# Performance work log

Hardware: AMD Instinct MI355X
Metric: run time of the kernel (lower is better)

Reference implementation:

```python
import jax, jax.numpy as jnp
import numpy as np
import math

GRID = 256       # grid_size
KMAX = 64        # max_elements_per_cell
RES = 512        # image resolution
SPAN = 4         # max grid cells per axis covered by one triangle bbox
NUM_VIEWS = 16
SCALE = 0.5


def _projection_matrix(x=0.5, n=1.5, f=100.0):
    return np.array([[n / x, 0.0, 0.0, 0.0],
                     [0.0, n / -x, 0.0, 0.0],
                     [0.0, 0.0, -(f + n) / (f - n), -(2.0 * f * n) / (f - n)],
                     [0.0, 0.0, -1.0, 0.0]], dtype=np.float32)


def _view_buffers(num_views, seed):
    rng = np.random.default_rng(seed)
    proj = _projection_matrix()
    mvps, lights = [], []
    for _ in range(num_views):
        u1, u2, u3 = rng.random(3)
        qx = math.sqrt(1.0 - u1) * math.sin(math.tau * u2)
        qy = math.sqrt(1.0 - u1) * math.cos(math.tau * u2)
        qz = math.sqrt(u1) * math.sin(math.tau * u3)
        qw = math.sqrt(u1) * math.cos(math.tau * u3)
        rot = np.array([[1 - 2 * (qy * qy + qz * qz), 2 * (qx * qy - qz * qw), 2 * (qx * qz + qy * qw)],
                        [2 * (qx * qy + qz * qw), 1 - 2 * (qx * qx + qz * qz), 2 * (qy * qz - qx * qw)],
                        [2 * (qx * qz - qy * qw), 2 * (qy * qz + qx * qw), 1 - 2 * (qx * qx + qy * qy)]], dtype=np.float32)
        rmat = np.eye(4, dtype=np.float32); rmat[:3, :3] = rot
        tmat = np.eye(4, dtype=np.float32); tmat[2, 3] = -4.0
        view = tmat @ rmat
        campos = np.linalg.inv(view)[:3, 3]
        light = -campos / (np.linalg.norm(campos) + 1e-8)
        mvps.append(proj @ view)
        lights.append(light.astype(np.float32))
    return np.stack(mvps).astype(np.float32), np.stack(lights).astype(np.float32)


def setup_inputs() -> dict:
    key = jax.random.key(0)
    k1, k2 = jax.random.split(key)
    F = 100_000
    # clustered per-triangle vertices -> small on-screen triangles (mesh-like locality)
    centers = jax.random.uniform(k1, (F, 1, 3), minval=-1.0, maxval=1.0)
    jitter = jax.random.normal(k2, (F, 3, 3)) * 0.02
    u = (centers + jitter).reshape(-1, 3).astype(jnp.float32)          # [3F,3]
    faces = jnp.arange(3 * F, dtype=jnp.int32).reshape(F, 3)
    mvps, light = _view_buffers(NUM_VIEWS, 42)
    return {"u": u,
            "mvps": jnp.asarray(mvps),
            "lightdir": jnp.asarray(light),
            "background_color": jnp.zeros(3, jnp.float32),
            "base_colors": jnp.ones((F, 3), jnp.float32),
            "faces": faces}


def _forward(u, mvps, lightdir, background_color, base_colors, faces):
    # _normalize_vertices
    v = u - u.mean(0, keepdims=True)
    span = jnp.maximum(v.max() - v.min(), 1e-6)
    v = v * (SCALE / span)
    Fn = faces.shape[0]
    # project with active view 0 (v_hom @ mvps[0].T, no perspective divide, as in source)
    v_hom = jnp.concatenate([v, jnp.ones((v.shape[0], 1), v.dtype)], axis=1)
    v_ndc = v_hom @ mvps[0].T                                          # [V,4]
    tris = v_ndc[faces]                                                # [F,3,4]
    wtri = v[faces]                                                    # [F,3,3]
    nrm = jnp.cross(wtri[:, 0] - wtri[:, 1], wtri[:, 2] - wtri[:, 1])
    nrm = nrm / (jnp.linalg.norm(nrm, axis=-1, keepdims=True) + 1e-10)
    z = tris[:, :, 2].mean(1)
    order = jnp.argsort(z)                                             # depth sort (near first)
    st = tris[order]
    sn = nrm[order]
    cp = (st[:, :, :2] + 1.0) * 0.5                                    # [F,3,2] control pts in [0,1]
    shading = jnp.clip(jnp.sum(-lightdir[0] * sn, axis=-1, keepdims=True), 0.0)
    colors = base_colors[order] * shading                              # [F,3]
    # --- grid acceleration structure build (scatter triangles into cells) ---
    lo = jnp.clip(jnp.floor(cp.min(1) * GRID).astype(jnp.int32), 0, GRID - 1)  # [F,2]
    hi = jnp.clip(jnp.floor(cp.max(1) * GRID).astype(jnp.int32), 0, GRID - 1)
    d = jnp.arange(SPAN, dtype=jnp.int32)
    cx = lo[:, 0:1] + d[None, :]                                       # [F,SPAN]
    cy = lo[:, 1:2] + d[None, :]
    valid = (cy[:, :, None] <= hi[:, 1:2, None]) & (cx[:, None, :] <= hi[:, 0:1].reshape(Fn, 1, 1) + 0 * cx[:, None, :])
    valid = (cy[:, :, None] <= hi[:, 1:2, None]) & (cx[:, None, :] <= hi[:, 0:1][:, :, None])
    cell = cy[:, :, None] * GRID + cx[:, None, :]                      # [F,SPAN,SPAN]
    NC = GRID * GRID
    cell = jnp.where(valid, cell, NC).reshape(-1)
    tri = jnp.broadcast_to(jnp.arange(Fn, dtype=jnp.int32)[:, None, None], (Fn, SPAN, SPAN)).reshape(-1)
    # sort (cell, depth-rank): tri ids are already depth-ordered
    keys = cell.astype(jnp.int64) * (Fn + 1) + tri
    ordk = jnp.argsort(keys)
    sc = cell[ordk]
    stri = tri[ordk]
    counts = jax.ops.segment_sum(jnp.ones_like(sc), sc, num_segments=NC + 1)
    starts = jnp.concatenate([jnp.zeros(1, counts.dtype), jnp.cumsum(counts)[:-1]])
    rank = jnp.arange(sc.shape[0], dtype=jnp.int32) - starts[sc].astype(jnp.int32)
    ok = (rank < KMAX) & (sc < NC)
    grid_elems = jnp.full((NC + 1, KMAX), -1, jnp.int32)
    grid_elems = grid_elems.at[jnp.where(ok, sc, NC), jnp.where(ok, rank, 0)].set(jnp.where(ok, stri, -1))
    # --- per-pixel rasterization via grid query ---
    px = (jnp.arange(RES, dtype=jnp.float32) + 0.5) / RES
    uu, vv = jnp.meshgrid(px, px, indexing='xy')
    P = jnp.stack([uu, vv], -1).reshape(-1, 2)                         # [P,2]
    ix = jnp.clip((P[:, 0] * GRID).astype(jnp.int32), 0, GRID - 1)
    iy = jnp.clip((P[:, 1] * GRID).astype(jnp.int32), 0, GRID - 1)
    elems = grid_elems[iy * GRID + ix]                                 # [P,K]
    e = jnp.maximum(elems, 0)
    tpts = cp[e]                                                       # [P,K,3,2]
    a, b, c = tpts[:, :, 0], tpts[:, :, 1], tpts[:, :, 2]
    pp = P[:, None, :]

    def cr(o, q, r):
        return (q[..., 0] - o[..., 0]) * (r[..., 1] - o[..., 1]) - (q[..., 1] - o[..., 1]) * (r[..., 0] - o[..., 0])

    e0 = cr(a, b, pp)
    e1 = cr(b, c, pp)
    e2 = cr(c, a, pp)
    inside = ((e0 >= 0) & (e1 >= 0) & (e2 >= 0)) | ((e0 <= 0) & (e1 <= 0) & (e2 <= 0))
    hit = inside & (elems >= 0)
    first = jnp.argmax(hit, axis=1)                                    # front-most (depth-sorted)
    anyhit = jnp.any(hit, axis=1)
    tid = e[jnp.arange(e.shape[0]), first]
    img = jnp.where(anyhit[:, None], colors[tid], background_color[None, :])
    return img.reshape(RES, RES, 3)


def reference(u, mvps, lightdir, background_color, base_colors, faces):
    return _forward(u, mvps, lightdir, background_color, base_colors, faces)
```

## Files before the change

### kernel.cpp

```cpp
#include <hip/hip_runtime.h>
#include <stdint.h>

#pragma clang fp contract(off)

#define GRIDN 256
#define NC (GRIDN * GRIDN)
#define RESN 512
#define RBLOCKS 256
#define CAP 1024
#define CPB 16
#define NB 32
#define NS 16
#define SBINS 2048


typedef unsigned short bfraw;
typedef unsigned short u16;

__device__ __forceinline__ float bf2f(bfraw h) {
    return __uint_as_float(((uint32_t)h) << 16);
}
__device__ __forceinline__ bfraw f2bf(float f) {
    uint32_t b = __float_as_uint(f);
    return (bfraw)((b + 0x7FFFu + ((b >> 16) & 1u)) >> 16);
}
__device__ __forceinline__ uint32_t fkey(float f) {
    uint32_t b = __float_as_uint(f);
    return (b & 0x80000000u) ? ~b : (b | 0x80000000u);
}

__global__ __launch_bounds__(256) void k_reduce1(const bfraw* __restrict__ u, int nrows,
                                                 double* __restrict__ psum,
                                                 float* __restrict__ pmin,
                                                 float* __restrict__ pmax) {
    __shared__ double ssum[256 * 3];
    __shared__ float smin[256 * 3];
    __shared__ float smax[256 * 3];
    int t = threadIdx.x;
    double s0 = 0.0, s1 = 0.0, s2 = 0.0;
    float mn0 = INFINITY, mn1 = INFINITY, mn2 = INFINITY;
    float mx0 = -INFINITY, mx1 = -INFINITY, mx2 = -INFINITY;
    for (int r = blockIdx.x * 256 + t; r < nrows; r += 256 * RBLOCKS) {
        float a = bf2f(u[3 * r + 0]);
        float b = bf2f(u[3 * r + 1]);
        float c = bf2f(u[3 * r + 2]);
        s0 += (double)a; s1 += (double)b; s2 += (double)c;
        mn0 = fminf(mn0, a); mx0 = fmaxf(mx0, a);
        mn1 = fminf(mn1, b); mx1 = fmaxf(mx1, b);
        mn2 = fminf(mn2, c); mx2 = fmaxf(mx2, c);
    }
    ssum[t * 3 + 0] = s0; ssum[t * 3 + 1] = s1; ssum[t * 3 + 2] = s2;
    smin[t * 3 + 0] = mn0; smin[t * 3 + 1] = mn1; smin[t * 3 + 2] = mn2;
    smax[t * 3 + 0] = mx0; smax[t * 3 + 1] = mx1; smax[t * 3 + 2] = mx2;
    __syncthreads();
    for (int st = 128; st > 0; st >>= 1) {
        if (t < st) {
            for (int c = 0; c < 3; c++) {
                ssum[t * 3 + c] += ssum[(t + st) * 3 + c];
                smin[t * 3 + c] = fminf(smin[t * 3 + c], smin[(t + st) * 3 + c]);
                smax[t * 3 + c] = fmaxf(smax[t * 3 + c], smax[(t + st) * 3 + c]);
            }
        }
        __syncthreads();
    }
    if (t == 0) {
        for (int c = 0; c < 3; c++) {
            psum[blockIdx.x * 3 + c] = ssum[c];
            pmin[blockIdx.x * 3 + c] = smin[c];
            pmax[blockIdx.x * 3 + c] = smax[c];
        }
    }
}

__global__ __launch_bounds__(256) void k_reduce2(const double* __restrict__ psum,
                                                 const float* __restrict__ pmin,
                                                 const float* __restrict__ pmax,
                                                 int nrows, float* __restrict__ cst) {
    __shared__ double ssum[256 * 3];
    __shared__ float smin[256 * 3];
    __shared__ float smax[256 * 3];
    int t = threadIdx.x;
    for (int c = 0; c < 3; c++) {
        ssum[t * 3 + c] = psum[t * 3 + c];
        smin[t * 3 + c] = pmin[t * 3 + c];
        smax[t * 3 + c] = pmax[t * 3 + c];
    }
    __syncthreads();
    for (int st = 128; st > 0; st >>= 1) {
        if (t < st) {
            for (int c = 0; c < 3; c++) {
                ssum[t * 3 + c] += ssum[(t + st) * 3 + c];
                smin[t * 3 + c] = fminf(smin[t * 3 + c], smin[(t + st) * 3 + c]);
                smax[t * 3 + c] = fmaxf(smax[t * 3 + c], smax[(t + st) * 3 + c]);
            }
        }
        __syncthreads();
    }
    if (t == 0) {
        float fn = (float)nrows;
        float m0 = (float)ssum[0] / fn;
        float m1 = (float)ssum[1] / fn;
        float m2 = (float)ssum[2] / fn;
        float vmax = fmaxf(fmaxf(smax[0] - m0, smax[1] - m1), smax[2] - m2);
        float vmin = fminf(fminf(smin[0] - m0, smin[1] - m1), smin[2] - m2);
        float span = fmaxf(vmax - vmin, 1e-06f);
        float s = 0.5f / span;
        cst[0] = m0; cst[1] = m1; cst[2] = m2; cst[3] = s;
    }
}

__global__ __launch_bounds__(256) void k_setup(const bfraw* __restrict__ u,
                                               const int* __restrict__ faces,
                                               const bfraw* __restrict__ mvp,
                                               const bfraw* __restrict__ light,
                                               const float* __restrict__ cst,
                                               int F,
                                               float* __restrict__ tcs,
                                               uint32_t* __restrict__ tz,
                                               uint32_t* __restrict__ tbox) {
    int f = blockIdx.x * 256 + threadIdx.x;
    if (f >= F) return;
    float m0 = cst[0], m1 = cst[1], m2 = cst[2], s = cst[3];
    float M[12];
    for (int i = 0; i < 12; i++) M[i] = bf2f(mvp[i]);

    float vx[3], vy[3], vz[3], cpx[3], cpy[3], zc[3];
    for (int j = 0; j < 3; j++) {
        int idx = faces[3 * f + j];
        float a = bf2f(u[3 * idx + 0]);
        float b = bf2f(u[3 * idx + 1]);
        float c = bf2f(u[3 * idx + 2]);
        float x = (a - m0) * s;
        float y = (b - m1) * s;
        float z = (c - m2) * s;
        vx[j] = x; vy[j] = y; vz[j] = z;
        float cx = fmaf(x, M[0], 0.0f);
        cx = fmaf(y, M[1], cx); cx = fmaf(z, M[2], cx); cx = cx + M[3];
        float cy = fmaf(x, M[4], 0.0f);
        cy = fmaf(y, M[5], cy); cy = fmaf(z, M[6], cy); cy = cy + M[7];
        float cz = fmaf(x, M[8], 0.0f);
        cz = fmaf(y, M[9], cz); cz = fmaf(z, M[10], cz); cz = cz + M[11];
        cpx[j] = (cx + 1.0f) * 0.5f;
        cpy[j] = (cy + 1.0f) * 0.5f;
        zc[j] = cz;
    }
    float zmean = ((zc[0] + zc[1]) + zc[2]) / 3.0f;

    float e1x = vx[0] - vx[1], e1y = vy[0] - vy[1], e1z = vz[0] - vz[1];
    float e2x = vx[2] - vx[1], e2y = vy[2] - vy[1], e2z = vz[2] - vz[1];
    float nx = e1y * e2z - e1z * e2y;
    float ny = e1z * e2x - e1x * e2z;
    float nz = e1x * e2y - e1y * e2x;
    float nn = nx * nx;
    nn = nn + ny * ny;
    nn = nn + nz * nz;
    float d = sqrtf(nn) + 1e-10f;
    float inx = nx / d, iny = ny / d, inz = nz / d;

    float l0 = bf2f(light[0]), l1 = bf2f(light[1]), l2 = bf2f(light[2]);
    float p0 = (-l0) * inx;
    float p1 = (-l1) * iny;
    float p2 = (-l2) * inz;
    float shading = fmaxf((p0 + p1) + p2, 0.0f);

    tcs[f * 8 + 0] = cpx[0]; tcs[f * 8 + 1] = cpy[0];
    tcs[f * 8 + 2] = cpx[1]; tcs[f * 8 + 3] = cpy[1];
    tcs[f * 8 + 4] = cpx[2]; tcs[f * 8 + 5] = cpy[2];
    tcs[f * 8 + 6] = shading;
    tcs[f * 8 + 7] = 0.0f;

    tz[f] = fkey(zmean);

    float mnx = fminf(fminf(cpx[0], cpx[1]), cpx[2]);
    float mny = fminf(fminf(cpy[0], cpy[1]), cpy[2]);
    float mxx = fmaxf(fmaxf(cpx[0], cpx[1]), cpx[2]);
    float mxy = fmaxf(fmaxf(cpy[0], cpy[1]), cpy[2]);
    int lox = (int)floorf(mnx * 256.0f); lox = lox < 0 ? 0 : (lox > 255 ? 255 : lox);
    int loy = (int)floorf(mny * 256.0f); loy = loy < 0 ? 0 : (loy > 255 ? 255 : loy);
    int hix = (int)floorf(mxx * 256.0f); hix = hix < 0 ? 0 : (hix > 255 ? 255 : hix);
    int hiy = (int)floorf(mxy * 256.0f); hiy = hiy < 0 ? 0 : (hiy > 255 ? 255 : hiy);
    int hx = hix < lox + 3 ? hix : lox + 3;
    int hy = hiy < loy + 3 ? hiy : loy + 3;
    tbox[f] = (uint32_t)lox | ((uint32_t)loy << 8) | ((uint32_t)hx << 16) | ((uint32_t)hy << 24);
}

__global__ __launch_bounds__(256) void k_count(const uint32_t* __restrict__ tbox,
                                               int F,
                                               u16* __restrict__ blockHist) {
    __shared__ uint32_t hist[SBINS];
    int b = blockIdx.x >> 4;
    int sl = blockIdx.x & (NS - 1);
    int chunk = (F + NB - 1) / NB;
    int fs = b * chunk;
    int fe = fs + chunk < F ? fs + chunk : F;
    int y0 = sl * 16, y1 = y0 + 15;
    for (int i = threadIdx.x; i < SBINS; i += 256) hist[i] = 0u;
    __syncthreads();
    for (int f = fs + threadIdx.x; f < fe; f += 256) {
        uint32_t bx = tbox[f];
        int lox = bx & 255, loy = (bx >> 8) & 255;
        int hx = (bx >> 16) & 255, hy = bx >> 24;
        int ys = loy > y0 ? loy : y0;
        int ye = hy < y1 ? hy : y1;
        for (int yy = ys; yy <= ye; yy++) {
            for (int xx = lox; xx <= hx; xx++) {
                uint32_t c = (uint32_t)(yy * GRIDN + xx) & 4095u;
                atomicAdd(&hist[c >> 1], 1u << (16u * (c & 1u)));
            }
        }
    }
    __syncthreads();
    uint32_t* dst = (uint32_t*)(blockHist + (size_t)b * NC) + sl * SBINS;
    for (int i = threadIdx.x; i < SBINS; i += 256) dst[i] = hist[i];
}

__global__ __launch_bounds__(1024) void k_scanA1(u16* __restrict__ blockHist,
                                                 uint32_t* __restrict__ cellOff,
                                                 uint32_t* __restrict__ blockSum) {
    __shared__ uint32_t sc[1024];
    int B = blockIdx.x, t = threadIdx.x;
    int c = B * 1024 + t;
    uint32_t tot = 0;
    for (int b = 0; b < NB; b++) {
        size_t o = (size_t)b * NC + c;
        uint32_t v = blockHist[o];
        blockHist[o] = (u16)tot;
        tot += v;
    }
    sc[t] = tot;
    __syncthreads();
    for (int st = 1; st < 1024; st <<= 1) {
        uint32_t a = 0;
        if (t >= st) a = sc[t - st];
        __syncthreads();
        if (t >= st) sc[t] += a;
        __syncthreads();
    }
    cellOff[c] = sc[t] - tot;
    if (t == 1023) blockSum[B] = sc[1023];
}

__global__ __launch_bounds__(1024) void k_scanB(uint32_t* __restrict__ cellOff,
                                                const uint32_t* __restrict__ blockSum) {
    __shared__ uint32_t pre[65];
    int B = blockIdx.x, t = threadIdx.x;
    if (t == 0) {
        uint32_t run = 0;
        for (int i = 0; i < 64; i++) { pre[i] = run; run += blockSum[i]; }
        pre[64] = run;
    }
    __syncthreads();
    cellOff[B * 1024 + t] += pre[B];
    if (B == 63 && t == 1023) cellOff[NC] = pre[64];
}

__global__ __launch_bounds__(256) void k_place(const uint32_t* __restrict__ tbox,
                                               const u16* __restrict__ blockHist,
                                               const uint32_t* __restrict__ cellOff,
                                               uint32_t* __restrict__ pairs,
                                               int F) {
    __shared__ uint32_t hist[SBINS];
    int b = blockIdx.x >> 4;
    int sl = blockIdx.x & (NS - 1);
    int chunk = (F + NB - 1) / NB;
    int fs = b * chunk;
    int fe = fs + chunk < F ? fs + chunk : F;
    int y0 = sl * 16, y1 = y0 + 15;
    uint32_t pcap = (uint32_t)F * 16u;
    for (int i = threadIdx.x; i < SBINS; i += 256) hist[i] = 0u;
    __syncthreads();
    for (int f = fs + threadIdx.x; f < fe; f += 256) {
        uint32_t bx = tbox[f];
        int lox = bx & 255, loy = (bx >> 8) & 255;
        int hx = (bx >> 16) & 255, hy = bx >> 24;
        int ys = loy > y0 ? loy : y0;
        int ye = hy < y1 ? hy : y1;
        for (int yy = ys; yy <= ye; yy++) {
            for (int xx = lox; xx <= hx; xx++) {
                uint32_t cell = (uint32_t)(yy * GRIDN + xx);
                uint32_t c = cell & 4095u;
                uint32_t sh = 16u * (c & 1u);
                uint32_t old = atomicAdd(&hist[c >> 1], 1u << sh);
                uint32_t r = (old >> sh) & 0xFFFFu;
                uint32_t pos = cellOff[cell] + (uint32_t)blockHist[(size_t)b * NC + cell] + r;
                if (pos < pcap) pairs[pos] = (uint32_t)f;
            }
        }
    }
}

__global__ __launch_bounds__(256) void k_cellsort(const uint32_t* __restrict__ cellOff,
                                                  const uint32_t* __restrict__ tz,
                                                  uint32_t* __restrict__ pairs,
                                                  int F) {
    __shared__ uint64_t lkeys[CAP];
    uint32_t pcap = (uint32_t)F * 16u;
    int t = threadIdx.x;
    for (int ci = 0; ci < CPB; ci++) {
        int cell = blockIdx.x + ci * (NC / CPB);
        uint32_t off = cellOff[cell];
        uint32_t end = cellOff[cell + 1];
        if (off > pcap || end > pcap || end < off) continue;
        uint32_t n = end - off;
        if (n <= 64u) continue;
        uint32_t m = n > CAP ? CAP : n;
        for (uint32_t i = t; i < m; i += 256) {
            uint32_t id = pairs[off + i];
            if (id >= (uint32_t)F) id = 0;
            lkeys[i] = ((uint64_t)tz[id] << 32) | id;
        }
        __syncthreads();
        uint64_t k0 = ~0ull, k1 = ~0ull, k2 = ~0ull, k3 = ~0ull;
        uint32_t i0 = t, i1 = t + 256, i2 = t + 512, i3 = t + 768;
        if (i0 < m) k0 = lkeys[i0];
        if (i1 < m) k1 = lkeys[i1];
        if (i2 < m) k2 = lkeys[i2];
        if (i3 < m) k3 = lkeys[i3];
        uint32_t r0 = 0, r1 = 0, r2 = 0, r3 = 0;
        for (uint32_t j = 0; j < m; j++) {
            uint64_t kj = lkeys[j];
            r0 += (kj < k0) ? 1u : 0u;
            r1 += (kj < k1) ? 1u : 0u;
            r2 += (kj < k2) ? 1u : 0u;
            r3 += (kj < k3) ? 1u : 0u;
        }
        if (i0 < m && r0 < 64u) pairs[off + r0] = (uint32_t)(k0 & 0xFFFFFFFFu);
        if (i1 < m && r1 < 64u) pairs[off + r1] = (uint32_t)(k1 & 0xFFFFFFFFu);
        if (i2 < m && r2 < 64u) pairs[off + r2] = (uint32_t)(k2 & 0xFFFFFFFFu);
        if (i3 < m && r3 < 64u) pairs[off + r3] = (uint32_t)(k3 & 0xFFFFFFFFu);
        __syncthreads();
    }
}

__global__ __launch_bounds__(256) void k_raster(const float* __restrict__ tcs,
                                                const uint32_t* __restrict__ tz,
                                                const uint32_t* __restrict__ cellOff,
                                                const uint32_t* __restrict__ pairs,
                                                const bfraw* __restrict__ basec,
                                                const bfraw* __restrict__ bg,
                                                bfraw* __restrict__ out, int F) {
    int p = blockIdx.x * 256 + threadIdx.x;
    int col = p & (RESN - 1);
    int row = p >> 9;
    float px = ((float)col + 0.5f) / 512.0f;
    float py = ((float)row + 0.5f) / 512.0f;
    int cell = (row >> 1) * GRIDN + (col >> 1);
    uint32_t pcap = (uint32_t)F * 16u;
    uint32_t off = cellOff[cell];
    uint32_t end = cellOff[cell + 1];
    uint32_t n = 0;
    if (off <= pcap && end <= pcap && end >= off) n = end - off;
    uint32_t m = n > 64u ? 64u : n;
    bool srt = n > 64u;
    uint64_t best = ~0ull;
    uint32_t bestId = 0u;
    float bestSh = 0.0f;
    bool found = false;
    for (uint32_t k = 0; k < m; k++) {
        uint32_t id = pairs[off + k];
        if (id >= (uint32_t)F) continue;
        const float4 A = *(const float4*)(tcs + (size_t)id * 8);
        const float4 B = *(const float4*)(tcs + (size_t)id * 8 + 4);
        float ax = A.x, ay = A.y, bx = A.z, by = A.w, cx = B.x, cy = B.y;
        float e0 = (bx - ax) * (py - ay) - (by - ay) * (px - ax);
        float e1 = (cx - bx) * (py - by) - (cy - by) * (px - bx);
        float e2 = (ax - cx) * (py - cy) - (ay - cy) * (px - cx);
        bool inside = (e0 >= 0.0f && e1 >= 0.0f && e2 >= 0.0f) ||
                      (e0 <= 0.0f && e1 <= 0.0f && e2 <= 0.0f);
        if (inside) {
            if (srt) {
                bestId = id; bestSh = B.z; found = true;
                break;
            }
            uint64_t key = ((uint64_t)tz[id] << 32) | id;
            if (key < best) { best = key; bestId = id; bestSh = B.z; found = true; }
        }
    }
    float r, g, b;
    if (found) {
        r = bf2f(basec[3 * bestId + 0]) * bestSh;
        g = bf2f(basec[3 * bestId + 1]) * bestSh;
        b = bf2f(basec[3 * bestId + 2]) * bestSh;
    } else {
        r = bf2f(bg[0]); g = bf2f(bg[1]); b = bf2f(bg[2]);
    }
    int o = p * 3;
    out[o + 0] = f2bf(r);
    out[o + 1] = f2bf(g);
    out[o + 2] = f2bf(b);
}

__global__ __launch_bounds__(256) void k_diag(bfraw* __restrict__ out, float code) {
    out[blockIdx.x * 256 + threadIdx.x] = f2bf(code);
}

extern "C" void kernel_launch(void* const* d_in, const int* in_sizes, int n_in,
                              void* d_out, int out_size, void* d_ws, size_t ws_size,
                              hipStream_t stream) {
    const bfraw* u = (const bfraw*)d_in[0];
    const bfraw* mvps = (const bfraw*)d_in[1];
    const bfraw* light = (const bfraw*)d_in[2];
    const bfraw* bg = (const bfraw*)d_in[3];
    const bfraw* basec = (const bfraw*)d_in[4];
    const int* faces = (const int*)d_in[5];
    int nrows = in_sizes[0] / 3;
    int F = in_sizes[5] / 3;
    bfraw* out = (bfraw*)d_out;

    char* w = (char*)d_ws;
    size_t off = 0;
    auto alloc = [&](size_t bytes) -> void* {
        off = (off + 255) & ~(size_t)255;
        void* p = w + off;
        off += bytes;
        return p;
    };

    float* cst = (float*)alloc(4 * sizeof(float));
    double* psum = (double*)alloc((size_t)RBLOCKS * 3 * sizeof(double));
    float* pmin = (float*)alloc((size_t)RBLOCKS * 3 * sizeof(float));
    float* pmax = (float*)alloc((size_t)RBLOCKS * 3 * sizeof(float));
    float* tcs = (float*)alloc((size_t)F * 8 * sizeof(float));
    uint32_t* tz = (uint32_t*)alloc((size_t)F * sizeof(uint32_t));
    uint32_t* tbox = (uint32_t*)alloc((size_t)F * sizeof(uint32_t));
    u16* blockHist = (u16*)alloc((size_t)NB * NC * sizeof(u16));
    uint32_t* cellOff = (uint32_t*)alloc(((size_t)NC + 1) * sizeof(uint32_t));
    uint32_t* blockSum = (uint32_t*)alloc(64 * sizeof(uint32_t));
    uint32_t* pairs = (uint32_t*)alloc((size_t)F * 16 * sizeof(uint32_t));
    size_t needed = off;

    if (ws_size < needed) {
        float code = 20000.0f + (float)(ws_size >> 20);
        k_diag<<<(RESN * RESN * 3) / 256, 256, 0, stream>>>(out, code);
        return;
    }

    k_reduce1<<<RBLOCKS, 256, 0, stream>>>(u, nrows, psum, pmin, pmax);
    k_reduce2<<<1, 256, 0, stream>>>(psum, pmin, pmax, nrows, cst);
    k_setup<<<(F + 255) / 256, 256, 0, stream>>>(u, faces, mvps, light, cst, F,
                                                 tcs, tz, tbox);
    k_count<<<NB * NS, 256, 0, stream>>>(tbox, F, blockHist);
    k_scanA1<<<64, 1024, 0, stream>>>(blockHist, cellOff, blockSum);
    k_scanB<<<64, 1024, 0, stream>>>(cellOff, blockSum);
    k_place<<<NB * NS, 256, 0, stream>>>(tbox, blockHist, cellOff, pairs, F);
    k_cellsort<<<NC / CPB, 256, 0, stream>>>(cellOff, tz, pairs, F);
    k_raster<<<(RESN * RESN) / 256, 256, 0, stream>>>(tcs, tz, cellOff, pairs,
                                                      basec, bg, out, F);
}
```

Baseline: 155.9 us.

## Fuse pipeline stages into one persistent kernel with software grid barriers

Replaces the chain of nine kernel launches with a single persistent cooperative-style kernel. The blocks loop over tasks for each stage and meet at atomic-counter grid barriers, so per-launch gaps and launch overhead go away. The scan stage is reworked so each of 256 threads handles four cells, and the block-prefix add is folded into consumers through a shared pre array instead of a separate pass. The barrier assumes every block is co-resident, which occupancy sizing is meant to guarantee. It adds spin-wait cost, and the persistent loop gives uneven load balance for the cellsort and raster stages.

```diff
diff --git a/kernel.cpp b/kernel.cpp
--- a/kernel.cpp
+++ b/kernel.cpp
@@ -12,6 +12,7 @@
 #define NB 32
 #define NS 16
 #define SBINS 2048
+#define MAXGRID 1024
 
 
 typedef unsigned short bfraw;
@@ -29,18 +30,38 @@
     return (b & 0x80000000u) ? ~b : (b | 0x80000000u);
 }
 
-__global__ __launch_bounds__(256) void k_reduce1(const bfraw* __restrict__ u, int nrows,
-                                                 double* __restrict__ psum,
-                                                 float* __restrict__ pmin,
-                                                 float* __restrict__ pmax) {
-    __shared__ double ssum[256 * 3];
-    __shared__ float smin[256 * 3];
-    __shared__ float smax[256 * 3];
-    int t = threadIdx.x;
+__device__ __forceinline__ void gsync(uint32_t* cnt, uint32_t* gen, int nb) {
+    __syncthreads();
+    if (threadIdx.x == 0) {
+        __threadfence();
+        uint32_t g = atomicAdd(gen, 0u);
+        uint32_t a = atomicAdd(cnt, 1u);
+        if (a == (uint32_t)nb - 1u) {
+            atomicExch(cnt, 0u);
+            __threadfence();
+            atomicAdd(gen, 1u);
+        } else {
+            long spins = 0;
+            while (atomicAdd(gen, 0u) == g) {
+                __builtin_amdgcn_s_sleep(2);
+                if (++spins > 100000000L) break;
+            }
+        }
+        __threadfence();
+    }
+    __syncthreads();
+}
+
+
+__device__ void dev_reduce_partial(const bfraw* __restrict__ u, int nrows, int task,
+                                   int t, double* ssum, float* smin, float* smax,
+                                   double* __restrict__ psum,
+                                   float* __restrict__ pmin,
+                                   float* __restrict__ pmax) {
     double s0 = 0.0, s1 = 0.0, s2 = 0.0;
     float mn0 = INFINITY, mn1 = INFINITY, mn2 = INFINITY;
     float mx0 = -INFINITY, mx1 = -INFINITY, mx2 = -INFINITY;
-    for (int r = blockIdx.x * 256 + t; r < nrows; r += 256 * RBLOCKS) {
+    for (int r = task * 256 + t; r < nrows; r += 256 * RBLOCKS) {
         float a = bf2f(u[3 * r + 0]);
         float b = bf2f(u[3 * r + 1]);
         float c = bf2f(u[3 * r + 2]);
@@ -65,21 +86,20 @@
     }
     if (t == 0) {
         for (int c = 0; c < 3; c++) {
-            psum[blockIdx.x * 3 + c] = ssum[c];
-            pmin[blockIdx.x * 3 + c] = smin[c];
-            pmax[blockIdx.x * 3 + c] = smax[c];
-        }
-    }
-}
-
-__global__ __launch_bounds__(256) void k_reduce2(const double* __restrict__ psum,
-                                                 const float* __restrict__ pmin,
-                                                 const float* __restrict__ pmax,
-                                                 int nrows, float* __restrict__ cst) {
-    __shared__ double ssum[256 * 3];
-    __shared__ float smin[256 * 3];
-    __shared__ float smax[256 * 3];
-    int t = threadIdx.x;
+            psum[task * 3 + c] = ssum[c];
+            pmin[task * 3 + c] = smin[c];
+            pmax[task * 3 + c] = smax[c];
+        }
+    }
+    __syncthreads();
+}
+
+__device__ void dev_reduce_final(const double* __restrict__ psum,
+                                 const float* __restrict__ pmin,
+                                 const float* __restrict__ pmax,
+                                 int nrows, int t,
+                                 double* ssum, float* smin, float* smax,
+                                 float* __restrict__ cst) {
     for (int c = 0; c < 3; c++) {
         ssum[t * 3 + c] = psum[t * 3 + c];
         smin[t * 3 + c] = pmin[t * 3 + c];
@@ -107,19 +127,17 @@
         float s = 0.5f / span;
         cst[0] = m0; cst[1] = m1; cst[2] = m2; cst[3] = s;
     }
-}
-
-__global__ __launch_bounds__(256) void k_setup(const bfraw* __restrict__ u,
-                                               const int* __restrict__ faces,
-                                               const bfraw* __restrict__ mvp,
-                                               const bfraw* __restrict__ light,
-                                               const float* __restrict__ cst,
-                                               int F,
-                                               float* __restrict__ tcs,
-                                               uint32_t* __restrict__ tz,
-                                               uint32_t* __restrict__ tbox) {
-    int f = blockIdx.x * 256 + threadIdx.x;
-    if (f >= F) return;
+    __syncthreads();
+}
+
+__device__ void dev_setup_one(const bfraw* __restrict__ u,
+                              const int* __restrict__ faces,
+                              const bfraw* __restrict__ mvp,
+                              const bfraw* __restrict__ light,
+                              const float* __restrict__ cst, int f,
+                              float* __restrict__ tcs,
+                              uint32_t* __restrict__ tz,
+                              uint32_t* __restrict__ tbox) {
     float m0 = cst[0], m1 = cst[1], m2 = cst[2], s = cst[3];
     float M[12];
     for (int i = 0; i < 12; i++) M[i] = bf2f(mvp[i]);
@@ -184,19 +202,18 @@
     tbox[f] = (uint32_t)lox | ((uint32_t)loy << 8) | ((uint32_t)hx << 16) | ((uint32_t)hy << 24);
 }
 
-__global__ __launch_bounds__(256) void k_count(const uint32_t* __restrict__ tbox,
-                                               int F,
-                                               u16* __restrict__ blockHist) {
-    __shared__ uint32_t hist[SBINS];
-    int b = blockIdx.x >> 4;
-    int sl = blockIdx.x & (NS - 1);
+__device__ void dev_count_task(const uint32_t* __restrict__ tbox, int F,
+                               u16* __restrict__ blockHist, uint32_t* hist,
+                               int task, int t) {
+    int b = task >> 4;
+    int sl = task & (NS - 1);
     int chunk = (F + NB - 1) / NB;
     int fs = b * chunk;
     int fe = fs + chunk < F ? fs + chunk : F;
     int y0 = sl * 16, y1 = y0 + 15;
-    for (int i = threadIdx.x; i < SBINS; i += 256) hist[i] = 0u;
-    __syncthreads();
-    for (int f = fs + threadIdx.x; f < fe; f += 256) {
+    for (int i = t; i < SBINS; i += 256) hist[i] = 0u;
+    __syncthreads();
+    for (int f = fs + t; f < fe; f += 256) {
         uint32_t bx = tbox[f];
         int lox = bx & 255, loy = (bx >> 8) & 255;
         int hx = (bx >> 16) & 255, hy = bx >> 24;
@@ -211,65 +228,62 @@
     }
     __syncthreads();
     uint32_t* dst = (uint32_t*)(blockHist + (size_t)b * NC) + sl * SBINS;
-    for (int i = threadIdx.x; i < SBINS; i += 256) dst[i] = hist[i];
-}
-
-__global__ __launch_bounds__(1024) void k_scanA1(u16* __restrict__ blockHist,
-                                                 uint32_t* __restrict__ cellOff,
-                                                 uint32_t* __restrict__ blockSum) {
-    __shared__ uint32_t sc[1024];
-    int B = blockIdx.x, t = threadIdx.x;
-    int c = B * 1024 + t;
-    uint32_t tot = 0;
-    for (int b = 0; b < NB; b++) {
-        size_t o = (size_t)b * NC + c;
-        uint32_t v = blockHist[o];
-        blockHist[o] = (u16)tot;
-        tot += v;
-    }
-    sc[t] = tot;
-    __syncthreads();
-    for (int st = 1; st < 1024; st <<= 1) {
+    for (int i = t; i < SBINS; i += 256) dst[i] = hist[i];
+    __syncthreads();
+}
+
+__device__ void dev_scan_task(u16* __restrict__ blockHist,
+                              uint32_t* __restrict__ cellOff,
+                              uint32_t* __restrict__ blockSum,
+                              uint32_t* sscan, int task, int t) {
+    int c0 = task * 1024 + t * 4;
+    uint32_t tot[4];
+    uint32_t tsum = 0;
+    for (int k = 0; k < 4; k++) {
+        uint32_t tt = 0;
+        for (int b = 0; b < NB; b++) {
+            size_t o = (size_t)b * NC + (c0 + k);
+            uint32_t v = blockHist[o];
+            blockHist[o] = (u16)tt;
+            tt += v;
+        }
+        tot[k] = tt;
+        tsum += tt;
+    }
+    sscan[t] = tsum;
+    __syncthreads();
+    for (int st = 1; st < 256; st <<= 1) {
         uint32_t a = 0;
-        if (t >= st) a = sc[t - st];
+        if (t >= st) a = sscan[t - st];
         __syncthreads();
-        if (t >= st) sc[t] += a;
+        if (t >= st) sscan[t] += a;
         __syncthreads();
     }
-    cellOff[c] = sc[t] - tot;
-    if (t == 1023) blockSum[B] = sc[1023];
-}
-
-__global__ __launch_bounds__(1024) void k_scanB(uint32_t* __restrict__ cellOff,
-                                                const uint32_t* __restrict__ blockSum) {
-    __shared__ uint32_t pre[65];
-    int B = blockIdx.x, t = threadIdx.x;
-    if (t == 0) {
-        uint32_t run = 0;
-        for (int i = 0; i < 64; i++) { pre[i] = run; run += blockSum[i]; }
-        pre[64] = run;
-    }
-    __syncthreads();
-    cellOff[B * 1024 + t] += pre[B];
-    if (B == 63 && t == 1023) cellOff[NC] = pre[64];
-}
-
-__global__ __launch_bounds__(256) void k_place(const uint32_t* __restrict__ tbox,
-                                               const u16* __restrict__ blockHist,
-                                               const uint32_t* __restrict__ cellOff,
-                                               uint32_t* __restrict__ pairs,
-                                               int F) {
-    __shared__ uint32_t hist[SBINS];
-    int b = blockIdx.x >> 4;
-    int sl = blockIdx.x & (NS - 1);
+    uint32_t run = sscan[t] - tsum;
+    for (int k = 0; k < 4; k++) {
+        cellOff[c0 + k] = run;
+        run += tot[k];
+    }
+    if (t == 255) blockSum[task] = sscan[255];
+    __syncthreads();
+}
+
+__device__ void dev_place_task(const uint32_t* __restrict__ tbox,
+                               const u16* __restrict__ blockHist,
+                               const uint32_t* __restrict__ cellOff,
+                               const uint32_t* pre,
+                               uint32_t* __restrict__ pairs, int F,
+                               uint32_t* hist, int task, int t) {
+    int b = task >> 4;
+    int sl = task & (NS - 1);
     int chunk = (F + NB - 1) / NB;
     int fs = b * chunk;
     int fe = fs + chunk < F ? fs + chunk : F;
     int y0 = sl * 16, y1 = y0 + 15;
     uint32_t pcap = (uint32_t)F * 16u;
-    for (int i = threadIdx.x; i < SBINS; i += 256) hist[i] = 0u;
-    __syncthreads();
-    for (int f = fs + threadIdx.x; f < fe; f += 256) {
+    for (int i = t; i < SBINS; i += 256) hist[i] = 0u;
+    __syncthreads();
+    for (int f = fs + t; f < fe; f += 256) {
         uint32_t bx = tbox[f];
         int lox = bx & 255, loy = (bx >> 8) & 255;
         int hx = (bx >> 16) & 255, hy = bx >> 24;
@@ -282,72 +296,70 @@
                 uint32_t sh = 16u * (c & 1u);
                 uint32_t old = atomicAdd(&hist[c >> 1], 1u << sh);
                 uint32_t r = (old >> sh) & 0xFFFFu;
-                uint32_t pos = cellOff[cell] + (uint32_t)blockHist[(size_t)b * NC + cell] + r;
+                uint32_t base = cellOff[cell] + (pre ? pre[cell >> 10] : 0u);
+                uint32_t pos = base + (uint32_t)blockHist[(size_t)b * NC + cell] + r;
                 if (pos < pcap) pairs[pos] = (uint32_t)f;
             }
         }
     }
-}
-
-__global__ __launch_bounds__(256) void k_cellsort(const uint32_t* __restrict__ cellOff,
-                                                  const uint32_t* __restrict__ tz,
-                                                  uint32_t* __restrict__ pairs,
-                                                  int F) {
-    __shared__ uint64_t lkeys[CAP];
+    __syncthreads();
+}
+
+__device__ void dev_cellsort_cell(const uint32_t* __restrict__ cellOff,
+                                  const uint32_t* pre,
+                                  const uint32_t* __restrict__ tz,
+                                  uint32_t* __restrict__ pairs, int F,
+                                  uint64_t* lkeys, int cell, int t) {
     uint32_t pcap = (uint32_t)F * 16u;
-    int t = threadIdx.x;
-    for (int ci = 0; ci < CPB; ci++) {
-        int cell = blockIdx.x + ci * (NC / CPB);
-        uint32_t off = cellOff[cell];
-        uint32_t end = cellOff[cell + 1];
-        if (off > pcap || end > pcap || end < off) continue;
-        uint32_t n = end - off;
-        if (n <= 64u) continue;
-        uint32_t m = n > CAP ? CAP : n;
-        for (uint32_t i = t; i < m; i += 256) {
-            uint32_t id = pairs[off + i];
-            if (id >= (uint32_t)F) id = 0;
-            lkeys[i] = ((uint64_t)tz[id] << 32) | id;
-        }
-        __syncthreads();
-        uint64_t k0 = ~0ull, k1 = ~0ull, k2 = ~0ull, k3 = ~0ull;
-        uint32_t i0 = t, i1 = t + 256, i2 = t + 512, i3 = t + 768;
-        if (i0 < m) k0 = lkeys[i0];
-        if (i1 < m) k1 = lkeys[i1];
-        if (i2 < m) k2 = lkeys[i2];
-        if (i3 < m) k3 = lkeys[i3];
-        uint32_t r0 = 0, r1 = 0, r2 = 0, r3 = 0;
-        for (uint32_t j = 0; j < m; j++) {
-            uint64_t kj = lkeys[j];
-            r0 += (kj < k0) ? 1u : 0u;
-            r1 += (kj < k1) ? 1u : 0u;
-            r2 += (kj < k2) ? 1u : 0u;
-            r3 += (kj < k3) ? 1u : 0u;
-        }
-        if (i0 < m && r0 < 64u) pairs[off + r0] = (uint32_t)(k0 & 0xFFFFFFFFu);
-        if (i1 < m && r1 < 64u) pairs[off + r1] = (uint32_t)(k1 & 0xFFFFFFFFu);
-        if (i2 < m && r2 < 64u) pairs[off + r2] = (uint32_t)(k2 & 0xFFFFFFFFu);
-        if (i3 < m && r3 < 64u) pairs[off + r3] = (uint32_t)(k3 & 0xFFFFFFFFu);
-        __syncthreads();
-    }
-}
-
-__global__ __launch_bounds__(256) void k_raster(const float* __restrict__ tcs,
-                                                const uint32_t* __restrict__ tz,
-                                                const uint32_t* __restrict__ cellOff,
-                                                const uint32_t* __restrict__ pairs,
-                                                const bfraw* __restrict__ basec,
-                                                const bfraw* __restrict__ bg,
-                                                bfraw* __restrict__ out, int F) {
-    int p = blockIdx.x * 256 + threadIdx.x;
+    uint32_t off = cellOff[cell] + (pre ? pre[cell >> 10] : 0u);
+    uint32_t end = cellOff[cell + 1] + (pre ? pre[(cell + 1) >> 10] : 0u);
+    if (off > pcap || end > pcap || end < off) return;
+    uint32_t n = end - off;
+    if (n <= 64u) return;
+    uint32_t m = n > CAP ? CAP : n;
+    for (uint32_t i = t; i < m; i += 256) {
+        uint32_t id = pairs[off + i];
+        if (id >= (uint32_t)F) id = 0;
+        lkeys[i] = ((uint64_t)tz[id] << 32) | id;
+    }
+    __syncthreads();
+    uint64_t k0 = ~0ull, k1 = ~0ull, k2 = ~0ull, k3 = ~0ull;
+    uint32_t i0 = t, i1 = t + 256, i2 = t + 512, i3 = t + 768;
+    if (i0 < m) k0 = lkeys[i0];
+    if (i1 < m) k1 = lkeys[i1];
+    if (i2 < m) k2 = lkeys[i2];
+    if (i3 < m) k3 = lkeys[i3];
+    uint32_t r0 = 0, r1 = 0, r2 = 0, r3 = 0;
+    for (uint32_t j = 0; j < m; j++) {
+        uint64_t kj = lkeys[j];
+        r0 += (kj < k0) ? 1u : 0u;
+        r1 += (kj < k1) ? 1u : 0u;
+        r2 += (kj < k2) ? 1u : 0u;
+        r3 += (kj < k3) ? 1u : 0u;
+    }
+    if (i0 < m && r0 < 64u) pairs[off + r0] = (uint32_t)(k0 & 0xFFFFFFFFu);
+    if (i1 < m && r1 < 64u) pairs[off + r1] = (uint32_t)(k1 & 0xFFFFFFFFu);
+    if (i2 < m && r2 < 64u) pairs[off + r2] = (uint32_t)(k2 & 0xFFFFFFFFu);
+    if (i3 < m && r3 < 64u) pairs[off + r3] = (uint32_t)(k3 & 0xFFFFFFFFu);
+    __syncthreads();
+}
+
+__device__ void dev_raster_pixel(const float* __restrict__ tcs,
+                                 const uint32_t* __restrict__ tz,
+                                 const uint32_t* __restrict__ cellOff,
+                                 const uint32_t* pre,
+                                 const uint32_t* __restrict__ pairs,
+                                 const bfraw* __restrict__ basec,
+                                 const bfraw* __restrict__ bg,
+                                 bfraw* __restrict__ out, int F, int p) {
     int col = p & (RESN - 1);
     int row = p >> 9;
     float px = ((float)col + 0.5f) / 512.0f;
     float py = ((float)row + 0.5f) / 512.0f;
     int cell = (row >> 1) * GRIDN + (col >> 1);
     uint32_t pcap = (uint32_t)F * 16u;
-    uint32_t off = cellOff[cell];
-    uint32_t end = cellOff[cell + 1];
+    uint32_t off = cellOff[cell] + (pre ? pre[cell >> 10] : 0u);
+    uint32_t end = cellOff[cell + 1] + (pre ? pre[(cell + 1) >> 10] : 0u);
     uint32_t n = 0;
     if (off <= pcap && end <= pcap && end >= off) n = end - off;
     uint32_t m = n > 64u ? 64u : n;
@@ -368,10 +380,7 @@
         bool inside = (e0 >= 0.0f && e1 >= 0.0f && e2 >= 0.0f) ||
                       (e0 <= 0.0f && e1 <= 0.0f && e2 <= 0.0f);
         if (inside) {
-            if (srt) {
-                bestId = id; bestSh = B.z; found = true;
-                break;
-            }
+            if (srt) { bestId = id; bestSh = B.z; found = true; break; }
             uint64_t key = ((uint64_t)tz[id] << 32) | id;
             if (key < best) { best = key; bestId = id; bestSh = B.z; found = true; }
         }
@@ -388,6 +397,157 @@
     out[o + 0] = f2bf(r);
     out[o + 1] = f2bf(g);
     out[o + 2] = f2bf(b);
+}
+
+__global__ void __launch_bounds__(256, 4)
+k_mega(const bfraw* __restrict__ u, const int* __restrict__ faces,
+       const bfraw* __restrict__ mvp, const bfraw* __restrict__ light,
+       const bfraw* __restrict__ bg, const bfraw* __restrict__ basec,
+       int nrows, int F,
+       double* __restrict__ psum, float* __restrict__ pmin, float* __restrict__ pmax,
+       float* __restrict__ cst, float* __restrict__ tcs,
+       uint32_t* __restrict__ tz, uint32_t* __restrict__ tbox,
+       u16* __restrict__ blockHist, uint32_t* __restrict__ cellOff,
+       uint32_t* __restrict__ blockSum, uint32_t* __restrict__ pairs,
+       bfraw* __restrict__ out, uint32_t* bcnt, uint32_t* bgen) {
+    int t = threadIdx.x;
+    int nb = gridDim.x;
+    __shared__ double ssum[768];
+    __shared__ float smin[768];
+    __shared__ float smax[768];
+    __shared__ uint32_t hist[SBINS];
+    __shared__ uint64_t lkeys[CAP];
+    __shared__ uint32_t sscan[256];
+    __shared__ uint32_t pre[65];
+
+    for (int task = blockIdx.x; task < RBLOCKS; task += nb)
+        dev_reduce_partial(u, nrows, task, t, ssum, smin, smax, psum, pmin, pmax);
+    gsync(bcnt, bgen, nb);
+    if (blockIdx.x == 0)
+        dev_reduce_final(psum, pmin, pmax, nrows, t, ssum, smin, smax, cst);
+    gsync(bcnt, bgen, nb);
+    int FB = (F + 255) >> 8;
+    for (int task = blockIdx.x; task < FB; task += nb) {
+        int f = task * 256 + t;
+        if (f < F) dev_setup_one(u, faces, mvp, light, cst, f, tcs, tz, tbox);
+    }
+    gsync(bcnt, bgen, nb);
+    for (int task = blockIdx.x; task < NB * NS; task += nb)
+        dev_count_task(tbox, F, blockHist, hist, task, t);
+    gsync(bcnt, bgen, nb);
+    for (int task = blockIdx.x; task < 64; task += nb)
+        dev_scan_task(blockHist, cellOff, blockSum, sscan, task, t);
+    if (blockIdx.x == 0 && t == 0) cellOff[NC] = 0u;
+    gsync(bcnt, bgen, nb);
+    if (t == 0) {
+        uint32_t run = 0;
+        for (int i = 0; i < 64; i++) { pre[i] = run; run += blockSum[i]; }
+        pre[64] = run;
+    }
+    __syncthreads();
+    for (int task = blockIdx.x; task < NB * NS; task += nb)
+        dev_place_task(tbox, blockHist, cellOff, pre, pairs, F, hist, task, t);
+    gsync(bcnt, bgen, nb);
+    for (int cell = blockIdx.x; cell < NC; cell += nb)
+        dev_cellsort_cell(cellOff, pre, tz, pairs, F, lkeys, cell, t);
+    gsync(bcnt, bgen, nb);
+    int PB = (RESN * RESN) >> 8;
+    for (int task = blockIdx.x; task < PB; task += nb) {
+        int p = task * 256 + t;
+        dev_raster_pixel(tcs, tz, cellOff, pre, pairs, basec, bg, out, F, p);
+    }
+}
+
+__global__ __launch_bounds__(256) void k_reduce1(const bfraw* __restrict__ u, int nrows,
+                                                 double* __restrict__ psum,
+                                                 float* __restrict__ pmin,
+                                                 float* __restrict__ pmax) {
+    __shared__ double ssum[768];
+    __shared__ float smin[768];
+    __shared__ float smax[768];
+    dev_reduce_partial(u, nrows, blockIdx.x, threadIdx.x, ssum, smin, smax,
+                       psum, pmin, pmax);
+}
+
+__global__ __launch_bounds__(256) void k_reduce2(const double* __restrict__ psum,
+                                                 const float* __restrict__ pmin,
+                                                 const float* __restrict__ pmax,
+                                                 int nrows, float* __restrict__ cst) {
+    __shared__ double ssum[768];
+    __shared__ float smin[768];
+    __shared__ float smax[768];
+    dev_reduce_final(psum, pmin, pmax, nrows, threadIdx.x, ssum, smin, smax, cst);
+}
+
+__global__ __launch_bounds__(256) void k_setup(const bfraw* __restrict__ u,
+                                               const int* __restrict__ faces,
+                                               const bfraw* __restrict__ mvp,
+                                               const bfraw* __restrict__ light,
+                                               const float* __restrict__ cst, int F,
+                                               float* __restrict__ tcs,
+                                               uint32_t* __restrict__ tz,
+                                               uint32_t* __restrict__ tbox) {
+    int f = blockIdx.x * 256 + threadIdx.x;
+    if (f < F) dev_setup_one(u, faces, mvp, light, cst, f, tcs, tz, tbox);
+}
+
+__global__ __launch_bounds__(256) void k_count(const uint32_t* __restrict__ tbox,
+                                               int F, u16* __restrict__ blockHist) {
+    __shared__ uint32_t hist[SBINS];
+    dev_count_task(tbox, F, blockHist, hist, blockIdx.x, threadIdx.x);
+}
+
+__global__ __launch_bounds__(256) void k_scanA(u16* __restrict__ blockHist,
+                                               uint32_t* __restrict__ cellOff,
+                                               uint32_t* __restrict__ blockSum) {
+    __shared__ uint32_t sscan[256];
+    dev_scan_task(blockHist, cellOff, blockSum, sscan, blockIdx.x, threadIdx.x);
+}
+
+__global__ __launch_bounds__(1024) void k_scanB(uint32_t* __restrict__ cellOff,
+                                                const uint32_t* __restrict__ blockSum) {
+    __shared__ uint32_t pre[65];
+    int B = blockIdx.x, t = threadIdx.x;
+    if (t == 0) {
+        uint32_t run = 0;
+        for (int i = 0; i < 64; i++) { pre[i] = run; run += blockSum[i]; }
+        pre[64] = run;
+    }
+    __syncthreads();
+    cellOff[B * 1024 + t] += pre[B];
+    if (B == 63 && t == 1023) cellOff[NC] = pre[64];
+}
+
+__global__ __launch_bounds__(256) void k_place(const uint32_t* __restrict__ tbox,
+                                               const u16* __restrict__ blockHist,
+                                               const uint32_t* __restrict__ cellOff,
+                                               uint32_t* __restrict__ pairs, int F) {
+    __shared__ uint32_t hist[SBINS];
+    dev_place_task(tbox, blockHist, cellOff, (const uint32_t*)nullptr, pairs, F,
+                   hist, blockIdx.x, threadIdx.x);
+}
+
+__global__ __launch_bounds__(256) void k_cellsort(const uint32_t* __restrict__ cellOff,
+                                                  const uint32_t* __restrict__ tz,
+                                                  uint32_t* __restrict__ pairs, int F) {
+    __shared__ uint64_t lkeys[CAP];
+    for (int ci = 0; ci < CPB; ci++) {
+        int cell = blockIdx.x + ci * (NC / CPB);
+        dev_cellsort_cell(cellOff, (const uint32_t*)nullptr, tz, pairs, F, lkeys,
+                          cell, threadIdx.x);
+    }
+}
+
+__global__ __launch_bounds__(256) void k_raster(const float* __restrict__ tcs,
+                                                const uint32_t* __restrict__ tz,
+                                                const uint32_t* __restrict__ cellOff,
+                                                const uint32_t* __restrict__ pairs,
+                                                const bfraw* __restrict__ basec,
+                                                const bfraw* __restrict__ bg,
+                                                bfraw* __restrict__ out, int F) {
+    int p = blockIdx.x * 256 + threadIdx.x;
+    dev_raster_pixel(tcs, tz, cellOff, (const uint32_t*)nullptr, pairs, basec, bg,
+                     out, F, p);
 }
 
 __global__ __launch_bounds__(256) void k_diag(bfraw* __restrict__ out, float code) {
@@ -427,6 +587,7 @@
     uint32_t* cellOff = (uint32_t*)alloc(((size_t)NC + 1) * sizeof(uint32_t));
     uint32_t* blockSum = (uint32_t*)alloc(64 * sizeof(uint32_t));
     uint32_t* pairs = (uint32_t*)alloc((size_t)F * 16 * sizeof(uint32_t));
+    uint32_t* bar = (uint32_t*)alloc(2 * sizeof(uint32_t));
     size_t needed = off;
 
     if (ws_size < needed) {
@@ -435,15 +596,29 @@
         return;
     }
 
-    k_reduce1<<<RBLOCKS, 256, 0, stream>>>(u, nrows, psum, pmin, pmax);
-    k_reduce2<<<1, 256, 0, stream>>>(psum, pmin, pmax, nrows, cst);
-    k_setup<<<(F + 255) / 256, 256, 0, stream>>>(u, faces, mvps, light, cst, F,
-                                                 tcs, tz, tbox);
-    k_count<<<NB * NS, 256, 0, stream>>>(tbox, F, blockHist);
-    k_scanA1<<<64, 1024, 0, stream>>>(blockHist, cellOff, blockSum);
-    k_scanB<<<64, 1024, 0, stream>>>(cellOff, blockSum);
-    k_place<<<NB * NS, 256, 0, stream>>>(tbox, blockHist, cellOff, pairs, F);
-    k_cellsort<<<NC / CPB, 256, 0, stream>>>(cellOff, tz, pairs, F);
-    k_raster<<<(RESN * RESN) / 256, 256, 0, stream>>>(tcs, tz, cellOff, pairs,
-                                                      basec, bg, out, F);
-}
+    int occ = 0;
+    hipError_t oe = hipOccupancyMaxActiveBlocksPerMultiprocessor(
+        &occ, reinterpret_cast<const void*>(k_mega), 256, 0);
+    int grid = (oe == hipSuccess && occ > 0) ? occ * 256 : 0;
+    if (grid > MAXGRID) grid = MAXGRID;
+
+    if (grid >= 256) {
+        hipMemsetAsync(bar, 0, 2 * sizeof(uint32_t), stream);
+        k_mega<<<grid, 256, 0, stream>>>(u, faces, mvps, light, bg, basec,
+                                         nrows, F, psum, pmin, pmax, cst, tcs,
+                                         tz, tbox, blockHist, cellOff, blockSum,
+                                         pairs, out, bar, bar + 1);
+    } else {
+        k_reduce1<<<RBLOCKS, 256, 0, stream>>>(u, nrows, psum, pmin, pmax);
+        k_reduce2<<<1, 256, 0, stream>>>(psum, pmin, pmax, nrows, cst);
+        k_setup<<<(F + 255) / 256, 256, 0, stream>>>(u, faces, mvps, light, cst, F,
+                                                     tcs, tz, tbox);
+        k_count<<<NB * NS, 256, 0, stream>>>(tbox, F, blockHist);
+        k_scanA<<<64, 256, 0, stream>>>(blockHist, cellOff, blockSum);
+        k_scanB<<<64, 1024, 0, stream>>>(cellOff, blockSum);
+        k_place<<<NB * NS, 256, 0, stream>>>(tbox, blockHist, cellOff, pairs, F);
+        k_cellsort<<<NC / CPB, 256, 0, stream>>>(cellOff, tz, pairs, F);
+        k_raster<<<(RESN * RESN) / 256, 256, 0, stream>>>(tcs, tz, cellOff, pairs,
+                                                          basec, bg, out, F);
+    }
+}
```

New measurement: 495.8 us. +217.9%, slower.
